# Kernel optimization log

Measured on AMD Instinct MI355X. Metric: run time of the kernel, lower is better.

The kernel has to match this reference:

```python
import jax, jax.numpy as jnp
import numpy as np

B = 2048
IN_FEATURES = 512
OUT_FEATURES = 32768
S = 64.0   # arcface default scale
M = 0.5    # arcface default margin
EPS = 1e-7


def _l2_normalize(x, axis=-1):
    # matches torch F.normalize(p=2, eps=1e-12)
    n = jnp.sqrt(jnp.sum(x * x, axis=axis, keepdims=True))
    return x / jnp.maximum(n, 1e-12)


def setup_inputs() -> dict:
    key = jax.random.key(0)
    k1, k2, k3 = jax.random.split(key, 3)
    features = jax.random.normal(k1, (B, IN_FEATURES), dtype=jnp.float32)
    y_true = jax.random.randint(k2, (B,), 0, OUT_FEATURES)
    # xavier_uniform_ for weight of shape (out, in)
    limit = float(np.sqrt(6.0 / (OUT_FEATURES + IN_FEATURES)))
    weight = jax.random.uniform(k3, (OUT_FEATURES, IN_FEATURES), dtype=jnp.float32,
                                minval=-limit, maxval=limit)
    return {"features": features, "y_true": y_true, "weight": weight}


def reference(features, y_true, weight):
    f = _l2_normalize(features)            # [B, D]
    w = _l2_normalize(weight)              # [C, D]
    wf = jnp.einsum('bd,cd->bc', f, w)     # [B, C] cosine logits
    tgt = wf[jnp.arange(wf.shape[0]), y_true]  # [B]
    # arcface margin transform
    numerator = S * jnp.cos(jnp.arccos(jnp.clip(tgt, -1.0 + EPS, 1.0 - EPS)) + M)
    # sum of exp(s*wf) over all non-target classes = full sum minus target term
    excl_sum = jnp.sum(jnp.exp(S * wf), axis=1) - jnp.exp(S * tgt)
    denominator = jnp.exp(numerator) + excl_sum
    L = numerator - jnp.log(denominator)
    return -jnp.mean(L)
```

## Files before the change

kernel.cpp:

```cpp
#include <hip/hip_runtime.h>
#include <hip/hip_bf16.h>
#include <math.h>


#define BN 2048
#define DK 512
#define CN 32768

typedef __attribute__((ext_vector_type(8))) short short8;
typedef __attribute__((ext_vector_type(4))) float floatx4;

__device__ inline float dot4(floatx4 a, floatx4 b) {
  return a.x * b.x + a.y * b.y + a.z * b.z + a.w * b.w;
}

__device__ inline unsigned short f2bf(float f) {
  union { float f; unsigned u; } a; a.f = f;
  unsigned u = a.u;
  return (unsigned short)((u + 0x7fffu + ((u >> 16) & 1u)) >> 16);
}

__device__ inline uint2 pack4(floatx4 v) {
  uint2 r;
  r.x = (unsigned)f2bf(v.x) | ((unsigned)f2bf(v.y) << 16);
  r.y = (unsigned)f2bf(v.z) | ((unsigned)f2bf(v.w) << 16);
  return r;
}

__device__ inline void async_ld16(const void* g, void* l) {
  __builtin_amdgcn_global_load_lds(
      (const __attribute__((address_space(1))) void*)g,
      (__attribute__((address_space(3))) void*)l, 16, 0, 0);
}

__global__ void prep_kernel(const float* __restrict__ feat,
                            const int* __restrict__ y,
                            const float* __restrict__ w,
                            __hip_bfloat16* __restrict__ fb,
                            __hip_bfloat16* __restrict__ wb,
                            float* __restrict__ tgt,
                            float* __restrict__ rowsum) {
  const int wave = threadIdx.x >> 6;
  const int l = threadIdx.x & 63;
  if (blockIdx.x < 8192) {
    const int row = blockIdx.x * 4 + wave;
    const floatx4* src = (const floatx4*)(w + (size_t)row * DK);
    floatx4 v0 = src[l];
    floatx4 v1 = src[64 + l];
    float s = dot4(v0, v0) + dot4(v1, v1);
#pragma unroll
    for (int off = 1; off < 64; off <<= 1) s += __shfl_xor(s, off, 64);
    const float scale = 1.0f / fmaxf(sqrtf(s), 1e-12f);
    v0 *= scale; v1 *= scale;
    uint2* db = (uint2*)(wb + (size_t)row * DK);
    db[l] = pack4(v0);
    db[64 + l] = pack4(v1);
  } else {
    const int i = (blockIdx.x - 8192) * 4 + wave;
    const floatx4* src = (const floatx4*)(feat + (size_t)i * DK);
    floatx4 v0 = src[l];
    floatx4 v1 = src[64 + l];
    const int cls = y[i];
    const floatx4* wr = (const floatx4*)(w + (size_t)cls * DK);
    floatx4 w0 = wr[l], w1 = wr[64 + l];
    float s  = dot4(v0, v0) + dot4(v1, v1);
    float d  = dot4(v0, w0) + dot4(v1, w1);
    float wn = dot4(w0, w0) + dot4(w1, w1);
#pragma unroll
    for (int off = 1; off < 64; off <<= 1) {
      s  += __shfl_xor(s, off, 64);
      d  += __shfl_xor(d, off, 64);
      wn += __shfl_xor(wn, off, 64);
    }
    const float fscale = 1.0f / fmaxf(sqrtf(s), 1e-12f);
    v0 *= fscale; v1 *= fscale;
    uint2* db = (uint2*)(fb + (size_t)i * DK);
    db[l] = pack4(v0);
    db[64 + l] = pack4(v1);
    if (l == 0) {
      tgt[i] = d * fscale / fmaxf(sqrtf(wn), 1e-12f);
      rowsum[i] = 0.0f;
    }
  }
}

__launch_bounds__(512, 4)
__global__ void gemm_exp_kernel(const __hip_bfloat16* __restrict__ fb,
                                const __hip_bfloat16* __restrict__ wb,
                                float* __restrict__ rowsum) {
  __shared__ short As[128 * 32];
  __shared__ short Bs[256 * 32];
  __shared__ float lsum[128];

  const int tid  = threadIdx.x;
  const int wave = tid >> 6;
  const int lane = tid & 63;
  const int tileM = blockIdx.x * 128;
  const int tileN = blockIdx.y * 256;

  const int wm = (wave >> 2) * 64;
  const int wn = (wave & 3) * 64;

  if (tid < 128) lsum[tid] = 0.0f;

  floatx4 acc[4][4];
#pragma unroll
  for (int mi = 0; mi < 4; ++mi)
#pragma unroll
    for (int ni = 0; ni < 4; ++ni)
      acc[mi][ni] = (floatx4){0.f, 0.f, 0.f, 0.f};

  const int sr = tid >> 2;
  const int sc = tid & 3;
  const int sg = sc ^ ((sr >> 1) & 3);
  const char* gA  = (const char*)fb + ((size_t)(tileM + sr)       * DK + sg * 8) * 2;
  const char* gB0 = (const char*)wb + ((size_t)(tileN + sr)       * DK + sg * 8) * 2;
  const char* gB1 = (const char*)wb + ((size_t)(tileN + 128 + sr) * DK + sg * 8) * 2;
  short* lA  = &As[wave * 512];
  short* lB0 = &Bs[wave * 512];
  short* lB1 = &Bs[4096 + wave * 512];

  const int mrow = lane & 15;
  const int gk   = lane >> 4;

  for (int kk = 0; kk < DK / 32; ++kk) {
    __syncthreads();
    async_ld16(gA,  lA);
    async_ld16(gB0, lB0);
    async_ld16(gB1, lB1);
    gA += 64; gB0 += 64; gB1 += 64;
    __syncthreads();

    short8 af[4], bf[4];
#pragma unroll
    for (int mi = 0; mi < 4; ++mi) {
      const int row = wm + mi * 16 + mrow;
      const int c = gk ^ ((row >> 1) & 3);
      af[mi] = *(const short8*)&As[row * 32 + c * 8];
    }
#pragma unroll
    for (int ni = 0; ni < 4; ++ni) {
      const int row = wn + ni * 16 + mrow;
      const int c = gk ^ ((row >> 1) & 3);
      bf[ni] = *(const short8*)&Bs[row * 32 + c * 8];
    }
#pragma unroll
    for (int mi = 0; mi < 4; ++mi)
#pragma unroll
      for (int ni = 0; ni < 4; ++ni)
        acc[mi][ni] = __builtin_amdgcn_mfma_f32_16x16x32_bf16(
            af[mi], bf[ni], acc[mi][ni], 0, 0, 0);
  }

  const int rowq = (lane >> 4) * 4;
#pragma unroll
  for (int mi = 0; mi < 4; ++mi) {
#pragma unroll
    for (int r = 0; r < 4; ++r) {
      float v = 0.f;
#pragma unroll
      for (int ni = 0; ni < 4; ++ni)
        v += __expf(64.0f * acc[mi][ni][r]);
      v += __shfl_xor(v, 1, 64);
      v += __shfl_xor(v, 2, 64);
      v += __shfl_xor(v, 4, 64);
      v += __shfl_xor(v, 8, 64);
      if ((lane & 15) == 0)
        atomicAdd(&lsum[wm + mi * 16 + rowq + r], v);
    }
  }
  __syncthreads();
  if (tid < 128)
    atomicAdd(&rowsum[tileM + tid], lsum[tid]);
}

__global__ void loss_kernel(const float* __restrict__ tgt,
                            const float* __restrict__ rowsum,
                            float* __restrict__ out) {
  __shared__ float wsum[8];
  const int t = threadIdx.x;
  float sum = 0.f;
  const float cM = 0.87758256189037271f;
  const float sM = 0.47942553860420301f;
  for (int i = t; i < BN; i += 512) {
    const float tg_raw = tgt[i];
    const float tg = fminf(fmaxf(tg_raw, -1.f + 1e-7f), 1.f - 1e-7f);
    const float num = 64.f * (tg * cM - sqrtf(fmaxf(1.f - tg * tg, 0.f)) * sM);
    const float den = expf(num) + rowsum[i] - expf(64.f * tg_raw);
    sum += num - logf(den);
  }
#pragma unroll
  for (int off = 1; off < 64; off <<= 1) sum += __shfl_xor(sum, off, 64);
  if ((t & 63) == 0) wsum[t >> 6] = sum;
  __syncthreads();
  if (t == 0) {
    float tot = 0.f;
#pragma unroll
    for (int k = 0; k < 8; ++k) tot += wsum[k];
    out[0] = -tot * (1.0f / (float)BN);
  }
}

extern "C" void kernel_launch(void* const* d_in, const int* in_sizes, int n_in,
                              void* d_out, int out_size, void* d_ws, size_t ws_size,
                              hipStream_t stream) {
  const float* features = (const float*)d_in[0];
  const int*   y_true   = (const int*)d_in[1];
  const float* weight   = (const float*)d_in[2];
  float* out = (float*)d_out;

  char* ws = (char*)d_ws;
  __hip_bfloat16* wb = (__hip_bfloat16*)(ws);
  __hip_bfloat16* fb = (__hip_bfloat16*)(ws + 33554432);
  float* tgt         = (float*)(ws + 35651584);
  float* rowsum      = (float*)(ws + 35659776);

  prep_kernel<<<8192 + 512, 256, 0, stream>>>(features, y_true, weight,
                                              fb, wb, tgt, rowsum);
  gemm_exp_kernel<<<dim3(BN / 128, CN / 256), 512, 0, stream>>>(fb, wb, rowsum);
  loss_kernel<<<1, 512, 0, stream>>>(tgt, rowsum, out);
}
```

Measured before the change: 186.7 us.

## Switch GEMM operands to FP8 with scaled MFMA 16x16x128

Normalized features and weights are quantized to FP8 (e4m3) instead of bf16, which halves operand memory traffic. The GEMM now uses the MX-scaled 16x16x128 f8f6f4 MFMA with neutral scales. The tile is restructured to 128x128 with 256 threads and a K step of 128, so only 4 iterations run, with a new XOR swizzle for LDS. FP8 precision raises error in logits that are then scaled by 64 before exp, which risks accuracy tolerance.

```diff
diff --git a/kernel.cpp b/kernel.cpp
--- a/kernel.cpp
+++ b/kernel.cpp
@@ -7,23 +7,16 @@
 #define DK 512
 #define CN 32768
 
-typedef __attribute__((ext_vector_type(8))) short short8;
 typedef __attribute__((ext_vector_type(4))) float floatx4;
+typedef __attribute__((ext_vector_type(8))) int int8v;
 
 __device__ inline float dot4(floatx4 a, floatx4 b) {
   return a.x * b.x + a.y * b.y + a.z * b.z + a.w * b.w;
 }
 
-__device__ inline unsigned short f2bf(float f) {
-  union { float f; unsigned u; } a; a.f = f;
-  unsigned u = a.u;
-  return (unsigned short)((u + 0x7fffu + ((u >> 16) & 1u)) >> 16);
-}
-
-__device__ inline uint2 pack4(floatx4 v) {
-  uint2 r;
-  r.x = (unsigned)f2bf(v.x) | ((unsigned)f2bf(v.y) << 16);
-  r.y = (unsigned)f2bf(v.z) | ((unsigned)f2bf(v.w) << 16);
+__device__ inline int pack_fp8x4(floatx4 v) {
+  int r = __builtin_amdgcn_cvt_pk_fp8_f32(v.x, v.y, 0, false);
+  r = __builtin_amdgcn_cvt_pk_fp8_f32(v.z, v.w, r, true);
   return r;
 }
 
@@ -36,8 +29,8 @@
 __global__ void prep_kernel(const float* __restrict__ feat,
                             const int* __restrict__ y,
                             const float* __restrict__ w,
-                            __hip_bfloat16* __restrict__ fb,
-                            __hip_bfloat16* __restrict__ wb,
+                            int* __restrict__ fb8,
+                            int* __restrict__ wb8,
                             float* __restrict__ tgt,
                             float* __restrict__ rowsum) {
   const int wave = threadIdx.x >> 6;
@@ -52,9 +45,9 @@
     for (int off = 1; off < 64; off <<= 1) s += __shfl_xor(s, off, 64);
     const float scale = 1.0f / fmaxf(sqrtf(s), 1e-12f);
     v0 *= scale; v1 *= scale;
-    uint2* db = (uint2*)(wb + (size_t)row * DK);
-    db[l] = pack4(v0);
-    db[64 + l] = pack4(v1);
+    int* db = wb8 + (size_t)row * 128;
+    db[l] = pack_fp8x4(v0);
+    db[64 + l] = pack_fp8x4(v1);
   } else {
     const int i = (blockIdx.x - 8192) * 4 + wave;
     const floatx4* src = (const floatx4*)(feat + (size_t)i * DK);
@@ -74,9 +67,9 @@
     }
     const float fscale = 1.0f / fmaxf(sqrtf(s), 1e-12f);
     v0 *= fscale; v1 *= fscale;
-    uint2* db = (uint2*)(fb + (size_t)i * DK);
-    db[l] = pack4(v0);
-    db[64 + l] = pack4(v1);
+    int* db = fb8 + (size_t)i * 128;
+    db[l] = pack_fp8x4(v0);
+    db[64 + l] = pack_fp8x4(v1);
     if (l == 0) {
       tgt[i] = d * fscale / fmaxf(sqrtf(wn), 1e-12f);
       rowsum[i] = 0.0f;
@@ -84,22 +77,22 @@
   }
 }
 
-__launch_bounds__(512, 4)
-__global__ void gemm_exp_kernel(const __hip_bfloat16* __restrict__ fb,
-                                const __hip_bfloat16* __restrict__ wb,
+__launch_bounds__(256, 3)
+__global__ void gemm_exp_kernel(const char* __restrict__ fb8,
+                                const char* __restrict__ wb8,
                                 float* __restrict__ rowsum) {
-  __shared__ short As[128 * 32];
-  __shared__ short Bs[256 * 32];
+  __shared__ char As[128 * 128];
+  __shared__ char Bs[128 * 128];
   __shared__ float lsum[128];
 
   const int tid  = threadIdx.x;
   const int wave = tid >> 6;
   const int lane = tid & 63;
   const int tileM = blockIdx.x * 128;
-  const int tileN = blockIdx.y * 256;
-
-  const int wm = (wave >> 2) * 64;
-  const int wn = (wave & 3) * 64;
+  const int tileN = blockIdx.y * 128;
+
+  const int wm = (wave >> 1) * 64;
+  const int wn = (wave & 1) * 64;
 
   if (tid < 128) lsum[tid] = 0.0f;
 
@@ -110,46 +103,56 @@
     for (int ni = 0; ni < 4; ++ni)
       acc[mi][ni] = (floatx4){0.f, 0.f, 0.f, 0.f};
 
-  const int sr = tid >> 2;
-  const int sc = tid & 3;
-  const int sg = sc ^ ((sr >> 1) & 3);
-  const char* gA  = (const char*)fb + ((size_t)(tileM + sr)       * DK + sg * 8) * 2;
-  const char* gB0 = (const char*)wb + ((size_t)(tileN + sr)       * DK + sg * 8) * 2;
-  const char* gB1 = (const char*)wb + ((size_t)(tileN + 128 + sr) * DK + sg * 8) * 2;
-  short* lA  = &As[wave * 512];
-  short* lB0 = &Bs[wave * 512];
-  short* lB1 = &Bs[4096 + wave * 512];
+  const int srow = (lane >> 3);
+  const int sch  = (lane & 7) ^ (srow & 7);
+  const char* gA[4];
+  const char* gB[4];
+#pragma unroll
+  for (int i = 0; i < 4; ++i) {
+    const int row = i * 32 + wave * 8 + srow;
+    gA[i] = fb8 + (size_t)(tileM + row) * DK + sch * 16;
+    gB[i] = wb8 + (size_t)(tileN + row) * DK + sch * 16;
+  }
+  char* lA = &As[wave * 1024];
+  char* lB = &Bs[wave * 1024];
 
   const int mrow = lane & 15;
-  const int gk   = lane >> 4;
-
-  for (int kk = 0; kk < DK / 32; ++kk) {
+  const int c0   = (lane >> 4) * 2;
+
+  for (int kk = 0; kk < 4; ++kk) {
     __syncthreads();
-    async_ld16(gA,  lA);
-    async_ld16(gB0, lB0);
-    async_ld16(gB1, lB1);
-    gA += 64; gB0 += 64; gB1 += 64;
+#pragma unroll
+    for (int i = 0; i < 4; ++i) {
+      async_ld16(gA[i], lA + i * 4096);
+      async_ld16(gB[i], lB + i * 4096);
+      gA[i] += 128; gB[i] += 128;
+    }
     __syncthreads();
 
-    short8 af[4], bf[4];
+    int8v af[4], bf[4];
 #pragma unroll
     for (int mi = 0; mi < 4; ++mi) {
       const int row = wm + mi * 16 + mrow;
-      const int c = gk ^ ((row >> 1) & 3);
-      af[mi] = *(const short8*)&As[row * 32 + c * 8];
+      const char* base = &As[row * 128];
+      *(int4*)&af[mi]       = *(const int4*)(base + ((c0     ^ (row & 7)) * 16));
+      *((int4*)&af[mi] + 1) = *(const int4*)(base + (((c0+1) ^ (row & 7)) * 16));
     }
 #pragma unroll
     for (int ni = 0; ni < 4; ++ni) {
       const int row = wn + ni * 16 + mrow;
-      const int c = gk ^ ((row >> 1) & 3);
-      bf[ni] = *(const short8*)&Bs[row * 32 + c * 8];
+      const char* base = &Bs[row * 128];
+      *(int4*)&bf[ni]       = *(const int4*)(base + ((c0     ^ (row & 7)) * 16));
+      *((int4*)&bf[ni] + 1) = *(const int4*)(base + (((c0+1) ^ (row & 7)) * 16));
     }
 #pragma unroll
     for (int mi = 0; mi < 4; ++mi)
 #pragma unroll
       for (int ni = 0; ni < 4; ++ni)
-        acc[mi][ni] = __builtin_amdgcn_mfma_f32_16x16x32_bf16(
-            af[mi], bf[ni], acc[mi][ni], 0, 0, 0);
+        acc[mi][ni] = __builtin_amdgcn_mfma_scale_f32_16x16x128_f8f6f4(
+            af[mi], bf[ni], acc[mi][ni],
+            0, 0,
+            0, 127,
+            0, 127);
   }
 
   const int rowq = (lane >> 4) * 4;
@@ -210,13 +213,13 @@
   float* out = (float*)d_out;
 
   char* ws = (char*)d_ws;
-  __hip_bfloat16* wb = (__hip_bfloat16*)(ws);
-  __hip_bfloat16* fb = (__hip_bfloat16*)(ws + 33554432);
-  float* tgt         = (float*)(ws + 35651584);
-  float* rowsum      = (float*)(ws + 35659776);
+  char* wb8    = ws;
+  char* fb8    = ws + 16777216;
+  float* tgt    = (float*)(ws + 17825792);
+  float* rowsum = (float*)(ws + 17833984);
 
   prep_kernel<<<8192 + 512, 256, 0, stream>>>(features, y_true, weight,
-                                              fb, wb, tgt, rowsum);
-  gemm_exp_kernel<<<dim3(BN / 128, CN / 256), 512, 0, stream>>>(fb, wb, rowsum);
+                                              (int*)fb8, (int*)wb8, tgt, rowsum);
+  gemm_exp_kernel<<<dim3(BN / 128, CN / 128), 256, 0, stream>>>(fb8, wb8, rowsum);
   loss_kernel<<<1, 512, 0, stream>>>(tgt, rowsum, out);
 }
```

Measured after the change: 318.6 us. 70.6% more time.
